# Optimization experiments

Hardware: AMD Instinct MI355X
Metric: run time of the kernel (lower is better)

The kernel has to match this reference:

```python
import jax, jax.numpy as jnp
import numpy as np

N_NODES = 32768
N_EDGES = 524288
NODE_DIM = 128
HIDDEN = 256
EDGE_DIM = 32


def setup_inputs() -> dict:
    key = jax.random.key(0)
    ks = jax.random.split(key, 12)
    s = 0.05
    return {
        "h": jax.random.normal(ks[0], (N_NODES, NODE_DIM), jnp.float32),
        "x": jax.random.normal(ks[1], (N_NODES, 3), jnp.float32) * 10.0,
        "edge_index": jax.random.randint(ks[2], (2, N_EDGES), 0, N_NODES, dtype=jnp.int32).astype(jnp.int64),
        "edge_dist": jax.random.uniform(ks[3], (N_EDGES,), jnp.float32) * 15.0,
        # edge_mlp: Linear(1, edge_dim) -> SiLU -> Linear(edge_dim, edge_dim)
        "We1": jax.random.normal(ks[4], (1, EDGE_DIM), jnp.float32) * s,
        "be1": jnp.zeros((EDGE_DIM,), jnp.float32),
        "We2": jax.random.normal(ks[5], (EDGE_DIM, EDGE_DIM), jnp.float32) * s,
        "be2": jnp.zeros((EDGE_DIM,), jnp.float32),
        # node_mlp: Linear(2*node+edge, hidden) -> SiLU -> Linear(hidden, node)
        "Wn1": jax.random.normal(ks[6], (2 * NODE_DIM + EDGE_DIM, HIDDEN), jnp.float32) * s,
        "bn1": jnp.zeros((HIDDEN,), jnp.float32),
        "Wn2": jax.random.normal(ks[7], (HIDDEN, NODE_DIM), jnp.float32) * s,
        "bn2": jnp.zeros((NODE_DIM,), jnp.float32),
        # coord_mlp: Linear(2*node+edge, hidden) -> SiLU -> Linear(hidden, 1, bias=False)
        "Wc1": jax.random.normal(ks[8], (2 * NODE_DIM + EDGE_DIM, HIDDEN), jnp.float32) * s,
        "bc1": jnp.zeros((HIDDEN,), jnp.float32),
        "Wc2": jax.random.normal(ks[9], (HIDDEN, 1), jnp.float32) * s,
    }


def reference(h, x, edge_index, edge_dist,
              We1, be1, We2, be2,
              Wn1, bn1, Wn2, bn2,
              Wc1, bc1, Wc2):
    src, dst = edge_index[0], edge_index[1]
    n_nodes = h.shape[0]

    # edge_mlp on scalar distances -> [E, edge_dim]
    edge_attr = jax.nn.silu(edge_dist[:, None] @ We1 + be1) @ We2 + be2

    # per-edge message input: [E, 2*node_dim + edge_dim]
    m_input = jnp.concatenate([h[src], h[dst], edge_attr], axis=-1)

    # node messages and scatter-add onto destination nodes
    m = jax.nn.silu(m_input @ Wn1 + bn1) @ Wn2 + bn2          # [E, node_dim]
    h_agg = jax.ops.segment_sum(m, dst, num_segments=n_nodes)  # [N, node_dim]

    # equivariant coordinate update along normalized edge direction
    coord_weight = jax.nn.silu(m_input @ Wc1 + bc1) @ Wc2      # [E, 1]
    dir_vec = x[src] - x[dst]                                  # [E, 3]
    dir_len = jnp.maximum(jnp.linalg.norm(dir_vec, axis=-1, keepdims=True), 1e-8)
    coord_update = coord_weight * (dir_vec / dir_len)          # [E, 3]
    x_agg = jax.ops.segment_sum(coord_update, dst, num_segments=n_nodes)

    return h + h_agg, x + x_agg
```

## Files before the change

### kernel.cpp

```cpp
#include <hip/hip_runtime.h>
#include <math.h>

#define N_NODES 32768
#define N_EDGES 524288
#define NODE_DIM 128
#define HIDDEN 256
#define EDGE_DIM 32
#define TE 64
#define ASTR 296
#define HSTR 264
#define MSTR 132

typedef __attribute__((ext_vector_type(8))) short bf16x8;
typedef __attribute__((ext_vector_type(16))) float f32x16;

__device__ __forceinline__ float silu_f(float v) {
    float e = __expf(-v);
    return v * __builtin_amdgcn_rcpf(1.0f + e);
}

__device__ __forceinline__ unsigned short f2bf_rne(float f) {
    union { float f; unsigned int u; } v; v.f = f;
    return (unsigned short)((v.u + 0x7fffu + ((v.u >> 16) & 1u)) >> 16);
}
__device__ __forceinline__ unsigned int pk_rne(float a, float b) {
    return (unsigned int)f2bf_rne(a) | ((unsigned int)f2bf_rne(b) << 16);
}
__device__ __forceinline__ unsigned int pkbf(float a, float b) {
    union { float f; unsigned int u; } ua, ub; ua.f = a; ub.f = b;
    return __builtin_amdgcn_perm(ub.u + 0x8000u, ua.u + 0x8000u, 0x07060302u);
}
__device__ __forceinline__ unsigned short f2bf_hu(float f) {
    union { float f; unsigned int u; } v; v.f = f;
    return (unsigned short)((v.u + 0x8000u) >> 16);
}

__device__ __forceinline__ int detect_is64(const void* ei, int t) {
    const unsigned int* ew = (const unsigned int*)ei;
    unsigned int hiw = ew[2 * (t & 63) + 1];
    return (__ballot(hiw != 0u) == 0ULL) ? 1 : 0;
}

#define WS_BIAS_OFF 1024
#define WS_W1S_OFF  69632
#define WS_W2S_OFF  364544
#define WS_CNT_OFF  430080
#define WS_CUR_OFF  561152
#define WS_PERM_OFF 692224
#define WS_PART_OFF 2789376
#define WS_HBF_OFF  2790400
#define WS_HBF_END  (WS_HBF_OFF + N_NODES * NODE_DIM * 2)

#define SEG_CNT  32768
#define SEG_W1S  147456
#define SEG_W2S  32768
#define SEG_BIAS 512
#define SEG_OUT  1073152
#define SEG_HBF  524288
#define PREP_TOT (SEG_CNT + SEG_W1S + SEG_W2S + SEG_BIAS + SEG_OUT + SEG_HBF)

__global__ void prep_all_kernel(const float* __restrict__ h, const float* __restrict__ x,
                                const float* __restrict__ We2, const float* __restrict__ be2,
                                const float* __restrict__ Wn1, const float* __restrict__ bn1,
                                const float* __restrict__ Wn2,
                                const float* __restrict__ Wc1, const float* __restrict__ bc1,
                                float* __restrict__ out, float* __restrict__ biasC,
                                unsigned short* __restrict__ W1s, unsigned short* __restrict__ W2s,
                                int* __restrict__ counts, unsigned short* __restrict__ hbf) {
    int i = blockIdx.x * 256 + threadIdx.x;
    if (i < SEG_CNT) { counts[i] = 0; return; }
    i -= SEG_CNT;
    if (i < SEG_W1S) {
        int jj = i & 7, ln = (i >> 3) & 63, rest = i >> 9;
        int step = rest % 18, tile = rest / 18;
        int n = tile * 32 + (ln & 31);
        int k = step * 16 + ((ln >> 5) * 8) + jj;
        float v;
        if (k < 256) {
            v = (n < 256) ? Wn1[k * 256 + n] : Wc1[k * 256 + (n - 256)];
        } else {
            int j = k - 256;
            float s = 0.0f;
            #pragma unroll 8
            for (int q = 0; q < 32; ++q)
                s += We2[j * 32 + q] * ((n < 256) ? Wn1[(256 + q) * 256 + n]
                                                  : Wc1[(256 + q) * 256 + (n - 256)]);
            v = s;
        }
        W1s[i] = f2bf_rne(v);
        return;
    }
    i -= SEG_W1S;
    if (i < SEG_W2S) {
        int jj = i & 7, ln = (i >> 3) & 63, rest = i >> 9;
        int step = rest & 15, tile = rest >> 4;
        int d = tile * 32 + (ln & 31);
        int k = step * 16 + ((ln >> 5) * 8) + jj;
        W2s[i] = f2bf_rne(Wn2[k * 128 + d]);
        return;
    }
    i -= SEG_W2S;
    if (i < SEG_BIAS) {
        int n = i;
        float s = (n < 256) ? bn1[n] : bc1[n - 256];
        #pragma unroll 8
        for (int q = 0; q < 32; ++q)
            s += be2[q] * ((n < 256) ? Wn1[(256 + q) * 256 + n]
                                     : Wc1[(256 + q) * 256 + (n - 256)]);
        biasC[n] = s;
        return;
    }
    i -= SEG_BIAS;
    if (i < SEG_OUT) {
        const int NH4 = N_NODES * NODE_DIM / 4;
        const float4* h4 = (const float4*)h;
        const float4* x4 = (const float4*)x;
        ((float4*)out)[i] = (i < NH4) ? h4[i] : x4[i - NH4];
        return;
    }
    i -= SEG_OUT;
    if (hbf != nullptr && i < SEG_HBF) {
        const float4* p = (const float4*)&h[i * 8];
        float4 v0 = p[0], v1 = p[1];
        uint4 o = make_uint4(pk_rne(v0.x, v0.y), pk_rne(v0.z, v0.w),
                             pk_rne(v1.x, v1.y), pk_rne(v1.z, v1.w));
        *(uint4*)&hbf[i * 8] = o;
    }
}

__global__ void hist_kernel(const void* __restrict__ ei, int* __restrict__ counts) {
    int is64 = detect_is64(ei, threadIdx.x);
    int e = blockIdx.x * 256 + threadIdx.x;
    int dst = is64 ? (int)((const long long*)ei)[N_EDGES + e]
                   : ((const int*)ei)[N_EDGES + e];
    atomicAdd(&counts[dst], 1);
}

__global__ __launch_bounds__(256)
void scanA_kernel(const int* __restrict__ counts, int* __restrict__ partials) {
    __shared__ int red[256];
    const int t = threadIdx.x;
    const int b = blockIdx.x;
    red[t] = counts[b * 256 + t];
    __syncthreads();
    #pragma unroll
    for (int s = 128; s > 0; s >>= 1) {
        if (t < s) red[t] += red[t + s];
        __syncthreads();
    }
    if (t == 0) partials[b] = red[0];
}

__global__ __launch_bounds__(256)
void scanC_kernel(const int* __restrict__ counts, const int* __restrict__ partials,
                  int* __restrict__ cursor) {
    __shared__ int pb[128];
    __shared__ int loc[256];
    const int t = threadIdx.x;
    const int b = blockIdx.x;
    if (t < 128) pb[t] = partials[t];
    int c = counts[b * 256 + t];
    loc[t] = c;
    __syncthreads();
    if (t == 0) {
        int s = 0;
        for (int j = 0; j < 128; ++j) { int v = pb[j]; pb[j] = s; s += v; }
    }
    #pragma unroll
    for (int d = 1; d < 256; d <<= 1) {
        int v = (t >= d) ? loc[t - d] : 0;
        __syncthreads();
        loc[t] += v;
        __syncthreads();
    }
    cursor[b * 256 + t] = pb[b] + loc[t] - c;
}

__global__ void place_kernel(const void* __restrict__ ei,
                             int* __restrict__ cursor, int* __restrict__ perm) {
    int is64 = detect_is64(ei, threadIdx.x);
    int e = blockIdx.x * 256 + threadIdx.x;
    int dst = is64 ? (int)((const long long*)ei)[N_EDGES + e]
                   : ((const int*)ei)[N_EDGES + e];
    int pos = atomicAdd(&cursor[dst], 1);
    perm[pos] = e;
}

__global__ __launch_bounds__(512, 4)
void egnn_mfma_kernel(const float* __restrict__ h, const float* __restrict__ x,
                      const void* __restrict__ ei, const float* __restrict__ dist,
                      const float* __restrict__ We1, const float* __restrict__ be1,
                      const float* __restrict__ bn2, const float* __restrict__ Wc2,
                      const float* __restrict__ biasC,
                      const unsigned short* __restrict__ W1s,
                      const unsigned short* __restrict__ W2s,
                      const int* __restrict__ perm,
                      const unsigned short* __restrict__ hbf,
                      float* __restrict__ out)
{
    __shared__ unsigned short smA[TE * ASTR];
    __shared__ int sidx[TE], didx[TE], eidx[TE];
    __shared__ float cw_s[TE];
    __shared__ float cxyz[3 * TE];

    unsigned short* smH = smA;
    float* smM = (float*)smA;

    const int t = threadIdx.x;
    const int lane = t & 63;
    const int wv = t >> 6;
    const int lo = lane & 31;
    const int hi = lane >> 5;
    const int ebase = blockIdx.x * TE;
    const int is64 = detect_is64(ei, t);

    if (t < 2 * TE) {
        int e = t & (TE - 1);
        int eid = perm[ebase + e];
        int which = t >> 6;
        long long pos = (long long)which * N_EDGES + eid;
        int idx = is64 ? (int)((const long long*)ei)[pos] : ((const int*)ei)[pos];
        if (which == 0) { sidx[e] = idx; eidx[e] = eid; }
        else didx[e] = idx;
        if (t < TE) cw_s[t] = 0.0f;
    }
    __syncthreads();

    if (hbf != nullptr) {
        #pragma unroll
        for (int it = 0; it < 4; ++it) {
            int id = it * 512 + t;
            int g = id & 15;
            int half = (id >> 4) & 1;
            int e = id >> 5;
            int node = half ? didx[e] : sidx[e];
            uint4 v = *(const uint4*)&hbf[node * NODE_DIM + 8 * g];
            *(uint4*)&smA[e * ASTR + half * NODE_DIM + 8 * g] = v;
        }
    } else {
        #pragma unroll
        for (int it = 0; it < 4; ++it) {
            int id = it * 512 + t;
            int g8 = id & 15;
            int half = (id >> 4) & 1;
            int e = id >> 5;
            int node = half ? didx[e] : sidx[e];
            const float4* p = (const float4*)&h[node * NODE_DIM + 8 * g8];
            float4 v0 = p[0], v1 = p[1];
            unsigned int a0 = pkbf(v0.x, v0.y), a1 = pkbf(v0.z, v0.w);
            unsigned int a2 = pkbf(v1.x, v1.y), a3 = pkbf(v1.z, v1.w);
            *(uint4*)&smA[e * ASTR + half * NODE_DIM + 8 * g8] = make_uint4(a0, a1, a2, a3);
        }
    }
    {
        int e = t >> 3;
        int j4 = (t & 7) * 4;
        float d = dist[eidx[e]];
        float s0 = silu_f(d * We1[j4 + 0] + be1[j4 + 0]);
        float s1 = silu_f(d * We1[j4 + 1] + be1[j4 + 1]);
        float s2 = silu_f(d * We1[j4 + 2] + be1[j4 + 2]);
        float s3 = silu_f(d * We1[j4 + 3] + be1[j4 + 3]);
        *(uint2*)&smA[e * ASTR + 2 * NODE_DIM + j4] = make_uint2(pkbf(s0, s1), pkbf(s2, s3));
    }
    __syncthreads();

    f32x16 a00, a01, a10, a11;
    {
        int nb = wv * 64 + lo;
        float b0 = biasC[nb], b1 = biasC[nb + 32];
        #pragma unroll
        for (int r = 0; r < 16; ++r) { a00[r] = b0; a01[r] = b1; a10[r] = b0; a11[r] = b1; }
    }
    {
        const int aoff0 = lo * ASTR + hi * 8;
        const int aoff1 = (32 + lo) * ASTR + hi * 8;
        const int TS = 18 * 64 * 8;
        const int base = ((wv * 2 * 18) * 64 + lane) * 8;
        bf16x8 b0s[3], b1s[3];
        b0s[0] = *(const bf16x8*)&W1s[base];
        b1s[0] = *(const bf16x8*)&W1s[base + TS];
        b0s[1] = *(const bf16x8*)&W1s[base + 512];
        b1s[1] = *(const bf16x8*)&W1s[base + 512 + TS];
        #pragma unroll
        for (int step = 0; step < 18; ++step) {
            const int cur = step % 3;
            if (step + 2 < 18) {
                const int pf = (step + 2) % 3;
                b0s[pf] = *(const bf16x8*)&W1s[base + (step + 2) * 512];
                b1s[pf] = *(const bf16x8*)&W1s[base + (step + 2) * 512 + TS];
            }
            bf16x8 f0 = *(const bf16x8*)&smA[aoff0 + step * 16];
            bf16x8 f1 = *(const bf16x8*)&smA[aoff1 + step * 16];
            a00 = __builtin_amdgcn_mfma_f32_32x32x16_bf16(f0, b0s[cur], a00, 0, 0, 0);
            a10 = __builtin_amdgcn_mfma_f32_32x32x16_bf16(f1, b0s[cur], a10, 0, 0, 0);
            a01 = __builtin_amdgcn_mfma_f32_32x32x16_bf16(f0, b1s[cur], a01, 0, 0, 0);
            a11 = __builtin_amdgcn_mfma_f32_32x32x16_bf16(f1, b1s[cur], a11, 0, 0, 0);
        }
    }
    __syncthreads();

    const int rowbase = 4 * hi;
    if (wv < 4) {
        int jb = wv * 64 + lo;
        #pragma unroll
        for (int r = 0; r < 16; ++r) {
            int er = (r & 3) + 8 * (r >> 2) + rowbase;
            unsigned short* row0 = &smH[er * HSTR + jb];
            unsigned short* row1 = &smH[(er + 32) * HSTR + jb];
            row0[0]  = f2bf_hu(silu_f(a00[r]));
            row0[32] = f2bf_hu(silu_f(a01[r]));
            row1[0]  = f2bf_hu(silu_f(a10[r]));
            row1[32] = f2bf_hu(silu_f(a11[r]));
        }
    } else {
        int nc = (wv - 4) * 64 + lo;
        float w0 = Wc2[nc], w1 = Wc2[nc + 32];
        float p0[16], p1[16];
        #pragma unroll
        for (int r = 0; r < 16; ++r) {
            p0[r] = silu_f(a00[r]) * w0 + silu_f(a01[r]) * w1;
            p1[r] = silu_f(a10[r]) * w0 + silu_f(a11[r]) * w1;
        }
        #pragma unroll
        for (int off = 1; off < 32; off <<= 1) {
            #pragma unroll
            for (int r = 0; r < 16; ++r) {
                p0[r] += __shfl_xor(p0[r], off);
                p1[r] += __shfl_xor(p1[r], off);
            }
        }
        if (lo == 0) {
            #pragma unroll
            for (int r = 0; r < 16; ++r) {
                int er = (r & 3) + 8 * (r >> 2) + rowbase;
                atomicAdd(&cw_s[er], p0[r]);
                atomicAdd(&cw_s[er + 32], p1[r]);
            }
        }
    }
    __syncthreads();

    if (t < TE) {
        int s = sidx[t], dn = didx[t];
        float dx = x[s * 3 + 0] - x[dn * 3 + 0];
        float dy = x[s * 3 + 1] - x[dn * 3 + 1];
        float dz = x[s * 3 + 2] - x[dn * 3 + 2];
        float len = fmaxf(sqrtf(dx * dx + dy * dy + dz * dz), 1e-8f);
        float w = cw_s[t] / len;
        cxyz[t] = w * dx; cxyz[TE + t] = w * dy; cxyz[2 * TE + t] = w * dz;
    }

    {
        const int et = wv >> 2;
        const int dt = wv & 3;
        const int d = dt * 32 + lo;
        f32x16 acc;
        float bb = bn2[d];
        #pragma unroll
        for (int r = 0; r < 16; ++r) acc[r] = bb;
        const int hoff = (et * 32 + lo) * HSTR + hi * 8;
        const int wb = ((dt * 16) * 64 + lane) * 8;
        bf16x8 bs[3];
        bs[0] = *(const bf16x8*)&W2s[wb];
        bs[1] = *(const bf16x8*)&W2s[wb + 512];
        #pragma unroll
        for (int step = 0; step < 16; ++step) {
            const int cur = step % 3;
            if (step + 2 < 16) {
                const int pf = (step + 2) % 3;
                bs[pf] = *(const bf16x8*)&W2s[wb + (step + 2) * 512];
            }
            bf16x8 af = *(const bf16x8*)&smH[hoff + step * 16];
            acc = __builtin_amdgcn_mfma_f32_32x32x16_bf16(af, bs[cur], acc, 0, 0, 0);
        }
        __syncthreads();
        #pragma unroll
        for (int r = 0; r < 16; ++r) {
            int er = et * 32 + (r & 3) + 8 * (r >> 2) + rowbase;
            smM[er * MSTR + d] = acc[r];
        }
    }
    __syncthreads();

    {
        const int g = t >> 5;
        const int d4 = (t & 31) * 4;
        for (int e0 = g; e0 < TE; e0 += 16) {
            if (e0 > 0 && didx[e0] == didx[e0 - 1]) continue;
            float4 s = *(const float4*)&smM[e0 * MSTR + d4];
            int er = e0 + 1;
            while (er < TE && didx[er] == didx[e0]) {
                float4 v = *(const float4*)&smM[er * MSTR + d4];
                s.x += v.x; s.y += v.y; s.z += v.z; s.w += v.w;
                ++er;
            }
            float* dp = &out[didx[e0] * NODE_DIM + d4];
            atomicAdd(dp + 0, s.x); atomicAdd(dp + 1, s.y);
            atomicAdd(dp + 2, s.z); atomicAdd(dp + 3, s.w);
        }
    }
    if (t < TE) {
        int e0 = t;
        if (e0 == 0 || didx[e0] != didx[e0 - 1]) {
            float sx = cxyz[e0], sy = cxyz[TE + e0], sz = cxyz[2 * TE + e0];
            int er = e0 + 1;
            while (er < TE && didx[er] == didx[e0]) {
                sx += cxyz[er]; sy += cxyz[TE + er]; sz += cxyz[2 * TE + er];
                ++er;
            }
            float* xo = out + N_NODES * NODE_DIM + didx[e0] * 3;
            atomicAdd(xo + 0, sx); atomicAdd(xo + 1, sy); atomicAdd(xo + 2, sz);
        }
    }
}

extern "C" void kernel_launch(void* const* d_in, const int* in_sizes, int n_in,
                              void* d_out, int out_size, void* d_ws, size_t ws_size,
                              hipStream_t stream) {
    const float* h    = (const float*)d_in[0];
    const float* x    = (const float*)d_in[1];
    const void*  ei   = d_in[2];
    const float* dist = (const float*)d_in[3];
    const float* We1  = (const float*)d_in[4];
    const float* be1  = (const float*)d_in[5];
    const float* We2  = (const float*)d_in[6];
    const float* be2  = (const float*)d_in[7];
    const float* Wn1  = (const float*)d_in[8];
    const float* bn1  = (const float*)d_in[9];
    const float* Wn2  = (const float*)d_in[10];
    const float* bn2  = (const float*)d_in[11];
    const float* Wc1  = (const float*)d_in[12];
    const float* bc1  = (const float*)d_in[13];
    const float* Wc2  = (const float*)d_in[14];
    float* out = (float*)d_out;

    float* biasC = (float*)((char*)d_ws + WS_BIAS_OFF);
    unsigned short* W1s = (unsigned short*)((char*)d_ws + WS_W1S_OFF);
    unsigned short* W2s = (unsigned short*)((char*)d_ws + WS_W2S_OFF);
    int* counts   = (int*)((char*)d_ws + WS_CNT_OFF);
    int* cursor   = (int*)((char*)d_ws + WS_CUR_OFF);
    int* perm     = (int*)((char*)d_ws + WS_PERM_OFF);
    int* partials = (int*)((char*)d_ws + WS_PART_OFF);
    unsigned short* hbf = (ws_size >= (size_t)WS_HBF_END)
                        ? (unsigned short*)((char*)d_ws + WS_HBF_OFF) : nullptr;

    prep_all_kernel<<<PREP_TOT / 256, 256, 0, stream>>>(
        h, x, We2, be2, Wn1, bn1, Wn2, Wc1, bc1,
        out, biasC, W1s, W2s, counts, hbf);

    hist_kernel<<<N_EDGES / 256, 256, 0, stream>>>(ei, counts);
    scanA_kernel<<<128, 256, 0, stream>>>(counts, partials);
    scanC_kernel<<<128, 256, 0, stream>>>(counts, partials, cursor);
    place_kernel<<<N_EDGES / 256, 256, 0, stream>>>(ei, cursor, perm);

    egnn_mfma_kernel<<<N_EDGES / TE, 512, 0, stream>>>(
        h, x, ei, dist, We1, be1, bn2, Wc2, biasC, W1s, W2s, perm, hbf, out);
}
```

Before: 480.4 us.

## Double edge tile to 128 with 1024-thread blocks and one N-tile per wave

Doubles the per-block edge tile to 128 edges and the block to 16 waves. Each wave now owns one 32-wide hidden column tile across four 32-edge row tiles, so each weight fragment is reused over more edges and global weight traffic per edge drops. The direction-vector computation is moved ahead of the first GEMM and later scaled by the coordinate weight. Weight prefetch depth grows to three steps. The costs are LDS roughly doubling per block, which cuts the number of resident blocks, and heavier register pressure at 1024 threads. The requested launch_bounds(1024,4) may not be satisfiable.

```diff
diff --git a/kernel.cpp b/kernel.cpp
--- a/kernel.cpp
+++ b/kernel.cpp
@@ -6,7 +6,7 @@
 #define NODE_DIM 128
 #define HIDDEN 256
 #define EDGE_DIM 32
-#define TE 64
+#define TE 128
 #define ASTR 296
 #define HSTR 264
 #define MSTR 132
@@ -186,7 +186,7 @@
     perm[pos] = e;
 }
 
-__global__ __launch_bounds__(512, 4)
+__global__ __launch_bounds__(1024, 4)
 void egnn_mfma_kernel(const float* __restrict__ h, const float* __restrict__ x,
                       const void* __restrict__ ei, const float* __restrict__ dist,
                       const float* __restrict__ We1, const float* __restrict__ be1,
@@ -217,19 +217,19 @@
     if (t < 2 * TE) {
         int e = t & (TE - 1);
         int eid = perm[ebase + e];
-        int which = t >> 6;
+        int which = t >> 7;
         long long pos = (long long)which * N_EDGES + eid;
         int idx = is64 ? (int)((const long long*)ei)[pos] : ((const int*)ei)[pos];
         if (which == 0) { sidx[e] = idx; eidx[e] = eid; }
         else didx[e] = idx;
-        if (t < TE) cw_s[t] = 0.0f;
-    }
+    }
+    if (t < TE) cw_s[t] = 0.0f;
     __syncthreads();
 
     if (hbf != nullptr) {
         #pragma unroll
         for (int it = 0; it < 4; ++it) {
-            int id = it * 512 + t;
+            int id = it * 1024 + t;
             int g = id & 15;
             int half = (id >> 4) & 1;
             int e = id >> 5;
@@ -240,7 +240,7 @@
     } else {
         #pragma unroll
         for (int it = 0; it < 4; ++it) {
-            int id = it * 512 + t;
+            int id = it * 1024 + t;
             int g8 = id & 15;
             int half = (id >> 4) & 1;
             int e = id >> 5;
@@ -262,92 +262,117 @@
         float s3 = silu_f(d * We1[j4 + 3] + be1[j4 + 3]);
         *(uint2*)&smA[e * ASTR + 2 * NODE_DIM + j4] = make_uint2(pkbf(s0, s1), pkbf(s2, s3));
     }
-    __syncthreads();
-
-    f32x16 a00, a01, a10, a11;
-    {
-        int nb = wv * 64 + lo;
-        float b0 = biasC[nb], b1 = biasC[nb + 32];
-        #pragma unroll
-        for (int r = 0; r < 16; ++r) { a00[r] = b0; a01[r] = b1; a10[r] = b0; a11[r] = b1; }
-    }
-    {
-        const int aoff0 = lo * ASTR + hi * 8;
-        const int aoff1 = (32 + lo) * ASTR + hi * 8;
-        const int TS = 18 * 64 * 8;
-        const int base = ((wv * 2 * 18) * 64 + lane) * 8;
-        bf16x8 b0s[3], b1s[3];
-        b0s[0] = *(const bf16x8*)&W1s[base];
-        b1s[0] = *(const bf16x8*)&W1s[base + TS];
-        b0s[1] = *(const bf16x8*)&W1s[base + 512];
-        b1s[1] = *(const bf16x8*)&W1s[base + 512 + TS];
-        #pragma unroll
-        for (int step = 0; step < 18; ++step) {
-            const int cur = step % 3;
-            if (step + 2 < 18) {
-                const int pf = (step + 2) % 3;
-                b0s[pf] = *(const bf16x8*)&W1s[base + (step + 2) * 512];
-                b1s[pf] = *(const bf16x8*)&W1s[base + (step + 2) * 512 + TS];
-            }
-            bf16x8 f0 = *(const bf16x8*)&smA[aoff0 + step * 16];
-            bf16x8 f1 = *(const bf16x8*)&smA[aoff1 + step * 16];
-            a00 = __builtin_amdgcn_mfma_f32_32x32x16_bf16(f0, b0s[cur], a00, 0, 0, 0);
-            a10 = __builtin_amdgcn_mfma_f32_32x32x16_bf16(f1, b0s[cur], a10, 0, 0, 0);
-            a01 = __builtin_amdgcn_mfma_f32_32x32x16_bf16(f0, b1s[cur], a01, 0, 0, 0);
-            a11 = __builtin_amdgcn_mfma_f32_32x32x16_bf16(f1, b1s[cur], a11, 0, 0, 0);
-        }
-    }
-    __syncthreads();
-
-    const int rowbase = 4 * hi;
-    if (wv < 4) {
-        int jb = wv * 64 + lo;
-        #pragma unroll
-        for (int r = 0; r < 16; ++r) {
-            int er = (r & 3) + 8 * (r >> 2) + rowbase;
-            unsigned short* row0 = &smH[er * HSTR + jb];
-            unsigned short* row1 = &smH[(er + 32) * HSTR + jb];
-            row0[0]  = f2bf_hu(silu_f(a00[r]));
-            row0[32] = f2bf_hu(silu_f(a01[r]));
-            row1[0]  = f2bf_hu(silu_f(a10[r]));
-            row1[32] = f2bf_hu(silu_f(a11[r]));
-        }
-    } else {
-        int nc = (wv - 4) * 64 + lo;
-        float w0 = Wc2[nc], w1 = Wc2[nc + 32];
-        float p0[16], p1[16];
-        #pragma unroll
-        for (int r = 0; r < 16; ++r) {
-            p0[r] = silu_f(a00[r]) * w0 + silu_f(a01[r]) * w1;
-            p1[r] = silu_f(a10[r]) * w0 + silu_f(a11[r]) * w1;
-        }
-        #pragma unroll
-        for (int off = 1; off < 32; off <<= 1) {
-            #pragma unroll
-            for (int r = 0; r < 16; ++r) {
-                p0[r] += __shfl_xor(p0[r], off);
-                p1[r] += __shfl_xor(p1[r], off);
-            }
-        }
-        if (lo == 0) {
-            #pragma unroll
-            for (int r = 0; r < 16; ++r) {
-                int er = (r & 3) + 8 * (r >> 2) + rowbase;
-                atomicAdd(&cw_s[er], p0[r]);
-                atomicAdd(&cw_s[er + 32], p1[r]);
-            }
-        }
-    }
-    __syncthreads();
-
     if (t < TE) {
         int s = sidx[t], dn = didx[t];
         float dx = x[s * 3 + 0] - x[dn * 3 + 0];
         float dy = x[s * 3 + 1] - x[dn * 3 + 1];
         float dz = x[s * 3 + 2] - x[dn * 3 + 2];
         float len = fmaxf(sqrtf(dx * dx + dy * dy + dz * dz), 1e-8f);
-        float w = cw_s[t] / len;
-        cxyz[t] = w * dx; cxyz[TE + t] = w * dy; cxyz[2 * TE + t] = w * dz;
+        float inv = 1.0f / len;
+        cxyz[t] = dx * inv; cxyz[TE + t] = dy * inv; cxyz[2 * TE + t] = dz * inv;
+    }
+    __syncthreads();
+
+    const int nt = wv;
+    f32x16 a0, a1, a2, a3;
+    {
+        float b = biasC[nt * 32 + lo];
+        #pragma unroll
+        for (int r = 0; r < 16; ++r) { a0[r] = b; a1[r] = b; a2[r] = b; a3[r] = b; }
+    }
+    {
+        const int ao = lo * ASTR + hi * 8;
+        const int base = ((nt * 18) * 64 + lane) * 8;
+        bf16x8 bs[4];
+        bs[0] = *(const bf16x8*)&W1s[base];
+        bs[1] = *(const bf16x8*)&W1s[base + 512];
+        bs[2] = *(const bf16x8*)&W1s[base + 1024];
+        #pragma unroll
+        for (int step = 0; step < 18; ++step) {
+            if (step + 3 < 18)
+                bs[(step + 3) & 3] = *(const bf16x8*)&W1s[base + (step + 3) * 512];
+            const int cur = step & 3;
+            bf16x8 f0 = *(const bf16x8*)&smA[ao +             step * 16];
+            bf16x8 f1 = *(const bf16x8*)&smA[ao + 32 * ASTR + step * 16];
+            bf16x8 f2 = *(const bf16x8*)&smA[ao + 64 * ASTR + step * 16];
+            bf16x8 f3 = *(const bf16x8*)&smA[ao + 96 * ASTR + step * 16];
+            a0 = __builtin_amdgcn_mfma_f32_32x32x16_bf16(f0, bs[cur], a0, 0, 0, 0);
+            a1 = __builtin_amdgcn_mfma_f32_32x32x16_bf16(f1, bs[cur], a1, 0, 0, 0);
+            a2 = __builtin_amdgcn_mfma_f32_32x32x16_bf16(f2, bs[cur], a2, 0, 0, 0);
+            a3 = __builtin_amdgcn_mfma_f32_32x32x16_bf16(f3, bs[cur], a3, 0, 0, 0);
+        }
+    }
+    __syncthreads();
+
+    const int rowbase = 4 * hi;
+    if (wv < 8) {
+        int jb = nt * 32 + lo;
+        #pragma unroll
+        for (int r = 0; r < 16; ++r) {
+            int er = (r & 3) + 8 * (r >> 2) + rowbase;
+            smH[(er     ) * HSTR + jb] = f2bf_hu(silu_f(a0[r]));
+            smH[(er + 32) * HSTR + jb] = f2bf_hu(silu_f(a1[r]));
+            smH[(er + 64) * HSTR + jb] = f2bf_hu(silu_f(a2[r]));
+            smH[(er + 96) * HSTR + jb] = f2bf_hu(silu_f(a3[r]));
+        }
+    } else {
+        int cc = (nt - 8) * 32 + lo;
+        float w = Wc2[cc];
+        float p[16];
+        #pragma unroll
+        for (int r = 0; r < 16; ++r) p[r] = silu_f(a0[r]) * w;
+        #pragma unroll
+        for (int off = 1; off < 32; off <<= 1) {
+            #pragma unroll
+            for (int r = 0; r < 16; ++r) p[r] += __shfl_xor(p[r], off);
+        }
+        if (lo == 0) {
+            #pragma unroll
+            for (int r = 0; r < 16; ++r)
+                atomicAdd(&cw_s[(r & 3) + 8 * (r >> 2) + rowbase], p[r]);
+        }
+        #pragma unroll
+        for (int r = 0; r < 16; ++r) p[r] = silu_f(a1[r]) * w;
+        #pragma unroll
+        for (int off = 1; off < 32; off <<= 1) {
+            #pragma unroll
+            for (int r = 0; r < 16; ++r) p[r] += __shfl_xor(p[r], off);
+        }
+        if (lo == 0) {
+            #pragma unroll
+            for (int r = 0; r < 16; ++r)
+                atomicAdd(&cw_s[32 + (r & 3) + 8 * (r >> 2) + rowbase], p[r]);
+        }
+        #pragma unroll
+        for (int r = 0; r < 16; ++r) p[r] = silu_f(a2[r]) * w;
+        #pragma unroll
+        for (int off = 1; off < 32; off <<= 1) {
+            #pragma unroll
+            for (int r = 0; r < 16; ++r) p[r] += __shfl_xor(p[r], off);
+        }
+        if (lo == 0) {
+            #pragma unroll
+            for (int r = 0; r < 16; ++r)
+                atomicAdd(&cw_s[64 + (r & 3) + 8 * (r >> 2) + rowbase], p[r]);
+        }
+        #pragma unroll
+        for (int r = 0; r < 16; ++r) p[r] = silu_f(a3[r]) * w;
+        #pragma unroll
+        for (int off = 1; off < 32; off <<= 1) {
+            #pragma unroll
+            for (int r = 0; r < 16; ++r) p[r] += __shfl_xor(p[r], off);
+        }
+        if (lo == 0) {
+            #pragma unroll
+            for (int r = 0; r < 16; ++r)
+                atomicAdd(&cw_s[96 + (r & 3) + 8 * (r >> 2) + rowbase], p[r]);
+        }
+    }
+    __syncthreads();
+
+    if (t < TE) {
+        float w = cw_s[t];
+        cxyz[t] *= w; cxyz[TE + t] *= w; cxyz[2 * TE + t] *= w;
     }
 
     {
@@ -360,18 +385,16 @@
         for (int r = 0; r < 16; ++r) acc[r] = bb;
         const int hoff = (et * 32 + lo) * HSTR + hi * 8;
         const int wb = ((dt * 16) * 64 + lane) * 8;
-        bf16x8 bs[3];
+        bf16x8 bs[4];
         bs[0] = *(const bf16x8*)&W2s[wb];
         bs[1] = *(const bf16x8*)&W2s[wb + 512];
+        bs[2] = *(const bf16x8*)&W2s[wb + 1024];
         #pragma unroll
         for (int step = 0; step < 16; ++step) {
-            const int cur = step % 3;
-            if (step + 2 < 16) {
-                const int pf = (step + 2) % 3;
-                bs[pf] = *(const bf16x8*)&W2s[wb + (step + 2) * 512];
-            }
+            if (step + 3 < 16)
+                bs[(step + 3) & 3] = *(const bf16x8*)&W2s[wb + (step + 3) * 512];
             bf16x8 af = *(const bf16x8*)&smH[hoff + step * 16];
-            acc = __builtin_amdgcn_mfma_f32_32x32x16_bf16(af, bs[cur], acc, 0, 0, 0);
+            acc = __builtin_amdgcn_mfma_f32_32x32x16_bf16(af, bs[step & 3], acc, 0, 0, 0);
         }
         __syncthreads();
         #pragma unroll
@@ -385,7 +408,7 @@
     {
         const int g = t >> 5;
         const int d4 = (t & 31) * 4;
-        for (int e0 = g; e0 < TE; e0 += 16) {
+        for (int e0 = g; e0 < TE; e0 += 32) {
             if (e0 > 0 && didx[e0] == didx[e0 - 1]) continue;
             float4 s = *(const float4*)&smM[e0 * MSTR + d4];
             int er = e0 + 1;
@@ -453,6 +476,6 @@
     scanC_kernel<<<128, 256, 0, stream>>>(counts, partials, cursor);
     place_kernel<<<N_EDGES / 256, 256, 0, stream>>>(ei, cursor, perm);
 
-    egnn_mfma_kernel<<<N_EDGES / TE, 512, 0, stream>>>(
+    egnn_mfma_kernel<<<N_EDGES / TE, 1024, 0, stream>>>(
         h, x, ei, dist, We1, be1, bn2, Wc2, biasC, W1s, W2s, perm, hbf, out);
 }
```

After: 598.3 us. 24.5% more time.
